# Optimization experiments

Hardware: AMD Instinct MI355X
Metric: run time of the kernel (lower is better)

Reference implementation:

```python
import jax, jax.numpy as jnp
import numpy as np

H, C, T = 4, 64, 6  # heads, per-head dim, num edge types


def segment_softmax(e, seg, n):
    # e: [E, H] logits, seg: [E] destination ids
    m = jax.ops.segment_max(e, seg, num_segments=n)
    m = jnp.where(jnp.isfinite(m), m, 0.0)
    w = jnp.exp(e - m[seg])
    s = jax.ops.segment_sum(w, seg, num_segments=n)
    return w / (s[seg] + 1e-16)


def gatv2(x_src, x_dst, ei, Wsrc, Wdst, att, b):
    # GATv2Conv (bipartite, add_self_loops=False, concat heads)
    n_dst = x_dst.shape[0]
    hs = (x_src @ Wsrc).reshape(x_src.shape[0], H, C)  # lin_l(x_src)
    hd = (x_dst @ Wdst).reshape(n_dst, H, C)            # lin_r(x_dst)
    src, dst = ei[0], ei[1]
    m = hs[src] + hd[dst]                                # [E,H,C]
    e = jnp.einsum('ehc,hc->eh', jax.nn.leaky_relu(m, 0.2), att)
    a = segment_softmax(e, dst, n_dst)                   # [E,H]
    out = jax.ops.segment_sum(a[:, :, None] * hs[src], dst, num_segments=n_dst)
    return out.reshape(n_dst, H * C) + b


def setup_inputs() -> dict:
    key = jax.random.key(0)
    ks = jax.random.split(key, 20)
    Npkg, N, Din, E, Dedge = 50000, 50000, 128, 200000, 8
    F = H * C  # 256
    K = T * Dedge  # num_clusters = 48 (forced by concat in subgraph_cls)
    s = 0.05
    return {
        'x_pkg': jax.random.normal(ks[0], (Npkg, Din), jnp.float32),
        'x_dst': jax.random.normal(ks[1], (T, N, Din), jnp.float32),
        'edge_attr': jax.random.uniform(ks[2], (T, E, Dedge), dtype=jnp.float32),
        'node_mask': jnp.ones((N,), jnp.float32),
        'W1_src': jax.random.normal(ks[3], (T, Din, F), jnp.float32) * s,
        'W1_dst': jax.random.normal(ks[4], (T, Din, F), jnp.float32) * s,
        'att1': jax.random.normal(ks[5], (T, H, C), jnp.float32) * s,
        'b1': jnp.zeros((T, F), jnp.float32),
        'W2_src': jax.random.normal(ks[6], (T, Din, F), jnp.float32) * s,
        'W2_dst': jax.random.normal(ks[7], (T, F, F), jnp.float32) * s,
        'att2': jax.random.normal(ks[8], (T, H, C), jnp.float32) * s,
        'b2': jnp.zeros((T, F), jnp.float32),
        'W_pool': jax.random.normal(ks[9], (F, K), jnp.float32) * s,
        'b_pool': jnp.zeros((K,), jnp.float32),
        'W_cls': jax.random.normal(ks[10], (F + 1, 1), jnp.float32) * s,
        'b_cls': jnp.zeros((1,), jnp.float32),
        'edge_index': jax.random.randint(ks[11], (T, 2, E), 0, N, dtype=jnp.int32),
        'batch': jnp.zeros((N,), jnp.int32),
    }


def reference(x_pkg, x_dst, edge_attr, node_mask, W1_src, W1_dst, att1, b1,
              W2_src, W2_dst, att2, b2, W_pool, b_pool, W_cls, b_cls,
              edge_index, batch):
    # node masking (edge_mask is all-ones -> bernoulli keeps every edge)
    xp = x_pkg * node_mask[:x_pkg.shape[0], None]
    outs = []
    for t in range(T):  # fixed set of 6 hetero edge types
        xd = x_dst[t] * node_mask[:x_dst.shape[1], None]
        h1 = jax.nn.relu(gatv2(xp, xd, edge_index[t], W1_src[t], W1_dst[t], att1[t], b1[t]))
        h2 = gatv2(xp, h1, edge_index[t], W2_src[t], W2_dst[t], att2[t], b2[t])
        outs.append(h2)
    h = outs[-1]  # forward keeps only the last node type's pooled embedding
    # DiffPool: soft assignment then pooled features
    s_assign = jax.nn.softmax(h @ W_pool + b_pool, axis=-1)  # [N, K]
    x_pooled = s_assign.T @ h                                 # [K, F]
    # global edge-attribute aggregation
    agg_edge = edge_attr.mean(axis=1).reshape(-1)             # [T*Dedge] == K
    feat = jnp.concatenate([x_pooled, agg_edge[:, None]], axis=-1)  # [K, F+1]
    return jax.nn.sigmoid(feat @ W_cls + b_cls)               # [K, 1]
```

## Files before the change

### kernel.cpp

```cpp
#include <hip/hip_runtime.h>
#include <math.h>

#define NN 50000
#define DIN 128
#define FDIM 256
#define EE 200000
#define TT 6
#define DE 8
#define KC 48
#define NB ((NN + 255)/256)

typedef __attribute__((ext_vector_type(8))) short bf16x8;
typedef __attribute__((ext_vector_type(8))) unsigned short u16x8;
typedef __attribute__((ext_vector_type(4))) float f32x4;

__device__ inline unsigned short f2b(float f){
  unsigned u = __float_as_uint(f);
  unsigned r = u + 0x7FFFu + ((u >> 16) & 1u);
  return (unsigned short)(r >> 16);
}
__device__ inline float b2f(unsigned short u){ return __uint_as_float(((unsigned)u) << 16); }

__global__ void zero_deg_agg(int* __restrict__ deg, int* __restrict__ aggE){
  int i = blockIdx.x*256 + threadIdx.x;
  if (i < NN) deg[i] = 0;
  if (i < 64) aggE[i] = 0;
}

__global__ void count_deg(const int* __restrict__ dst, int* __restrict__ deg){
  int i = blockIdx.x*256 + threadIdx.x;
  if (i < EE) atomicAdd(&deg[dst[i]], 1);
}

__global__ __launch_bounds__(256) void scan_blk(const int* __restrict__ deg, int* __restrict__ rp,
                                                int* __restrict__ bsum){
  __shared__ int sm[256];
  int i = blockIdx.x*256 + threadIdx.x;
  int v = (i < NN) ? deg[i] : 0;
  sm[threadIdx.x] = v;
  __syncthreads();
  #pragma unroll
  for (int off = 1; off < 256; off <<= 1){
    int t = (threadIdx.x >= (unsigned)off) ? sm[threadIdx.x - off] : 0;
    __syncthreads();
    sm[threadIdx.x] += t;
    __syncthreads();
  }
  if (i < NN) rp[i] = sm[threadIdx.x] - v;
  if (threadIdx.x == 255) bsum[blockIdx.x] = sm[255];
}

__global__ __launch_bounds__(256) void scan_sums(const int* __restrict__ bsum, int* __restrict__ boff){
  __shared__ int sm[256];
  int v = (threadIdx.x < NB) ? bsum[threadIdx.x] : 0;
  sm[threadIdx.x] = v;
  __syncthreads();
  #pragma unroll
  for (int off = 1; off < 256; off <<= 1){
    int t = (threadIdx.x >= (unsigned)off) ? sm[threadIdx.x - off] : 0;
    __syncthreads();
    sm[threadIdx.x] += t;
    __syncthreads();
  }
  if (threadIdx.x < NB) boff[threadIdx.x] = sm[threadIdx.x] - v;
}

__global__ __launch_bounds__(256) void scan_add(int* __restrict__ rp, const int* __restrict__ boff,
                                                int* __restrict__ cursor){
  int i = blockIdx.x*256 + threadIdx.x;
  if (i < NN){
    int r = rp[i] + boff[blockIdx.x];
    rp[i] = r;
    cursor[i] = r;
  }
  if (i == 0) rp[NN] = EE;
}

__global__ void scatter_edges(const int* __restrict__ src, const int* __restrict__ dst,
                              int* __restrict__ cursor, int* __restrict__ srt){
  int i = blockIdx.x*256 + threadIdx.x;
  if (i < EE){ int pos = atomicAdd(&cursor[dst[i]], 1); srt[pos] = src[i]; }
}

__global__ void cvt_wt_all(const float* __restrict__ W1s, const float* __restrict__ W2s,
                           const float* __restrict__ W1d, const float* __restrict__ W2d,
                           unsigned short* __restrict__ Wtall, unsigned short* __restrict__ Wt2d){
  int n = blockIdx.x;
  int which = blockIdx.y;
  if (which == 3){
    for (int k = threadIdx.x; k < FDIM; k += 256)
      Wt2d[(size_t)n*FDIM + k] = f2b(W2d[(size_t)k*256 + n]);
  } else {
    const float* W = (which == 0) ? W1s : (which == 1) ? W2s : W1d;
    unsigned short* o = Wtall + (size_t)which*256*DIN + (size_t)n*DIN;
    for (int k = threadIdx.x; k < DIN; k += 256)
      o[k] = f2b(W[(size_t)k*256 + n]);
  }
}

__global__ __launch_bounds__(256) void gemm_l1(const float* __restrict__ Apkg, const float* __restrict__ Adst,
                                               const unsigned short* __restrict__ Wtall,
                                               const float* __restrict__ mask,
                                               unsigned short* __restrict__ Chs1,
                                               unsigned short* __restrict__ Chs2,
                                               unsigned short* __restrict__ Chd1){
  __shared__ short Afull[128][136];
  __shared__ short Bl[128][56];
  int tid = threadIdx.x;
  int lane = tid & 63;
  int w = tid >> 6;
  int wm = w >> 1, wn = w & 1;
  int row0 = blockIdx.x * 128;
  int fr = lane & 15;
  int kb = lane >> 4;
  const float* A = blockIdx.y ? Adst : Apkg;
  #pragma unroll
  for (int p = 0; p < 8; p++){
    int idx = tid + p*256;
    int r = idx >> 4, ch = idx & 15;
    int gr = row0 + r;
    u16x8 o = (u16x8){0,0,0,0,0,0,0,0};
    if (gr < NN){
      float mv = mask[gr];
      const float* ap = A + (size_t)gr*DIN + ch*8;
      float4 a0 = *(const float4*)(ap);
      float4 a1 = *(const float4*)(ap + 4);
      o[0]=f2b(a0.x*mv); o[1]=f2b(a0.y*mv); o[2]=f2b(a0.z*mv); o[3]=f2b(a0.w*mv);
      o[4]=f2b(a1.x*mv); o[5]=f2b(a1.y*mv); o[6]=f2b(a1.z*mv); o[7]=f2b(a1.w*mv);
    }
    *(u16x8*)(&Afull[r][ch*8]) = o;
  }
  int ntile = blockIdx.y ? 2 : 4;
  #pragma unroll 1
  for (int t = 0; t < ntile; t++){
    int wsel = blockIdx.y ? 2 : (t >> 1);
    const unsigned short* Wt = Wtall + (size_t)wsel*256*DIN;
    unsigned short* Co = blockIdx.y ? Chd1 : ((t >> 1) ? Chs2 : Chs1);
    int col0 = (t & 1) * 128;
    f32x4 acc[4][4];
    #pragma unroll
    for (int i = 0; i < 4; i++)
      #pragma unroll
      for (int j = 0; j < 4; j++)
        acc[i][j] = (f32x4){0.f, 0.f, 0.f, 0.f};
    for (int k0 = 0; k0 < DIN; k0 += 32){
      bf16x8 rb[2];
      #pragma unroll
      for (int p = 0; p < 2; p++){
        int idx = tid + p*256;
        int r = idx >> 2, ch = idx & 3;
        rb[p] = *(const bf16x8*)(Wt + (size_t)(col0 + r)*DIN + k0 + ch*8);
      }
      __syncthreads();
      #pragma unroll
      for (int p = 0; p < 2; p++){
        int idx = tid + p*256;
        int r = idx >> 2, ch = idx & 3;
        *(bf16x8*)(&Bl[r][ch*8]) = rb[p];
      }
      __syncthreads();
      bf16x8 af[4], bfr[4];
      #pragma unroll
      for (int i = 0; i < 4; i++) af[i]  = *(const bf16x8*)(&Afull[wm*64 + i*16 + fr][k0 + kb*8]);
      #pragma unroll
      for (int j = 0; j < 4; j++) bfr[j] = *(const bf16x8*)(&Bl[wn*64 + j*16 + fr][kb*8]);
      #pragma unroll
      for (int i = 0; i < 4; i++)
        #pragma unroll
        for (int j = 0; j < 4; j++)
          acc[i][j] = __builtin_amdgcn_mfma_f32_16x16x32_bf16(af[i], bfr[j], acc[i][j], 0, 0, 0);
    }
    #pragma unroll
    for (int i = 0; i < 4; i++){
      #pragma unroll
      for (int q = 0; q < 4; q++){
        int grow = row0 + wm*64 + i*16 + kb*4 + q;
        if (grow < NN){
          #pragma unroll
          for (int j = 0; j < 4; j++)
            Co[(size_t)grow*256 + col0 + wn*64 + j*16 + fr] = f2b(acc[i][j][q]);
        }
      }
    }
  }
}

__global__ __launch_bounds__(256) void gemm_bf16(const short* __restrict__ A, const short* __restrict__ Wt,
                                                 unsigned short* __restrict__ Cb, int M, int K){
  __shared__ short Al[128][56];
  __shared__ short Bl[128][56];
  int tid = threadIdx.x;
  int lane = tid & 63;
  int w = tid >> 6;
  int wm = w >> 1, wn = w & 1;
  int row0 = blockIdx.x * 128, col0 = blockIdx.y * 128;
  int fr = lane & 15;
  int kb = lane >> 4;
  f32x4 acc[4][4];
  #pragma unroll
  for (int i = 0; i < 4; i++)
    #pragma unroll
    for (int j = 0; j < 4; j++)
      acc[i][j] = (f32x4){0.f, 0.f, 0.f, 0.f};

  for (int k0 = 0; k0 < K; k0 += 32){
    bf16x8 ra[2], rb[2];
    #pragma unroll
    for (int p = 0; p < 2; p++){
      int idx = tid + p*256;
      int r = idx >> 2, ch = idx & 3;
      int gr = row0 + r;
      if (gr < M) ra[p] = *(const bf16x8*)(A + (size_t)gr*K + k0 + ch*8);
      else        ra[p] = (bf16x8){0,0,0,0,0,0,0,0};
      rb[p] = *(const bf16x8*)(Wt + (size_t)(col0 + r)*K + k0 + ch*8);
    }
    __syncthreads();
    #pragma unroll
    for (int p = 0; p < 2; p++){
      int idx = tid + p*256;
      int r = idx >> 2, ch = idx & 3;
      *(bf16x8*)(&Al[r][ch*8]) = ra[p];
      *(bf16x8*)(&Bl[r][ch*8]) = rb[p];
    }
    __syncthreads();
    bf16x8 af[4], bfr[4];
    #pragma unroll
    for (int i = 0; i < 4; i++) af[i]  = *(const bf16x8*)(&Al[wm*64 + i*16 + fr][kb*8]);
    #pragma unroll
    for (int j = 0; j < 4; j++) bfr[j] = *(const bf16x8*)(&Bl[wn*64 + j*16 + fr][kb*8]);
    #pragma unroll
    for (int i = 0; i < 4; i++)
      #pragma unroll
      for (int j = 0; j < 4; j++)
        acc[i][j] = __builtin_amdgcn_mfma_f32_16x16x32_bf16(af[i], bfr[j], acc[i][j], 0, 0, 0);
  }
  #pragma unroll
  for (int i = 0; i < 4; i++){
    #pragma unroll
    for (int q = 0; q < 4; q++){
      int grow = row0 + wm*64 + i*16 + kb*4 + q;
      if (grow < M){
        #pragma unroll
        for (int j = 0; j < 4; j++)
          Cb[(size_t)grow*256 + col0 + wn*64 + j*16 + fr] = f2b(acc[i][j][q]);
      }
    }
  }
}

__global__ __launch_bounds__(256) void gat_fused(const int* __restrict__ rp, const int* __restrict__ srt,
                                                 const unsigned short* __restrict__ hs,
                                                 const unsigned short* __restrict__ hd,
                                                 const float* __restrict__ att, const float* __restrict__ bias,
                                                 unsigned short* __restrict__ outb, int do_relu){
  int n = blockIdx.x*4 + (threadIdx.x >> 6);
  int lane = threadIdx.x & 63;
  if (n >= NN) return;
  const float4 av = *(const float4*)(att + lane*4);
  ushort4 ud = *(const ushort4*)(hd + (size_t)n*256 + lane*4);
  float d0 = b2f(ud.x), d1 = b2f(ud.y), d2 = b2f(ud.z), d3 = b2f(ud.w);
  int beg = rp[n], end = rp[n+1];
  float4 acc = {0.f,0.f,0.f,0.f};
  float sw = 0.f;
  int i = beg;
  for (; i + 1 < end; i += 2){
    int sA = srt[i], sB = srt[i+1];
    ushort4 uA = *(const ushort4*)(hs + (size_t)sA*256 + lane*4);
    ushort4 uB = *(const ushort4*)(hs + (size_t)sB*256 + lane*4);
    float hA0 = b2f(uA.x), hA1 = b2f(uA.y), hA2 = b2f(uA.z), hA3 = b2f(uA.w);
    float hB0 = b2f(uB.x), hB1 = b2f(uB.y), hB2 = b2f(uB.z), hB3 = b2f(uB.w);
    float mA0 = hA0 + d0, mA1 = hA1 + d1, mA2 = hA2 + d2, mA3 = hA3 + d3;
    float mB0 = hB0 + d0, mB1 = hB1 + d1, mB2 = hB2 + d2, mB3 = hB3 + d3;
    mA0 = (mA0 > 0.f) ? mA0 : 0.2f*mA0;  mB0 = (mB0 > 0.f) ? mB0 : 0.2f*mB0;
    mA1 = (mA1 > 0.f) ? mA1 : 0.2f*mA1;  mB1 = (mB1 > 0.f) ? mB1 : 0.2f*mB1;
    mA2 = (mA2 > 0.f) ? mA2 : 0.2f*mA2;  mB2 = (mB2 > 0.f) ? mB2 : 0.2f*mB2;
    mA3 = (mA3 > 0.f) ? mA3 : 0.2f*mA3;  mB3 = (mB3 > 0.f) ? mB3 : 0.2f*mB3;
    float pA = mA0*av.x + mA1*av.y + mA2*av.z + mA3*av.w;
    float pB = mB0*av.x + mB1*av.y + mB2*av.z + mB3*av.w;
    #pragma unroll
    for (int msk = 8; msk > 0; msk >>= 1){
      pA += __shfl_xor(pA, msk);
      pB += __shfl_xor(pB, msk);
    }
    float wA = expf(fminf(pA, 80.f));
    float wB = expf(fminf(pB, 80.f));
    acc.x = fmaf(wA, hA0, fmaf(wB, hB0, acc.x));
    acc.y = fmaf(wA, hA1, fmaf(wB, hB1, acc.y));
    acc.z = fmaf(wA, hA2, fmaf(wB, hB2, acc.z));
    acc.w = fmaf(wA, hA3, fmaf(wB, hB3, acc.w));
    sw += wA + wB;
  }
  if (i < end){
    int s = srt[i];
    ushort4 uh = *(const ushort4*)(hs + (size_t)s*256 + lane*4);
    float h0 = b2f(uh.x), h1 = b2f(uh.y), h2 = b2f(uh.z), h3 = b2f(uh.w);
    float m0 = h0 + d0, m1 = h1 + d1, m2 = h2 + d2, m3 = h3 + d3;
    m0 = (m0 > 0.f) ? m0 : 0.2f*m0;
    m1 = (m1 > 0.f) ? m1 : 0.2f*m1;
    m2 = (m2 > 0.f) ? m2 : 0.2f*m2;
    m3 = (m3 > 0.f) ? m3 : 0.2f*m3;
    float p = m0*av.x + m1*av.y + m2*av.z + m3*av.w;
    #pragma unroll
    for (int msk = 8; msk > 0; msk >>= 1) p += __shfl_xor(p, msk);
    float wv = expf(fminf(p, 80.f));
    acc.x = fmaf(wv, h0, acc.x);
    acc.y = fmaf(wv, h1, acc.y);
    acc.z = fmaf(wv, h2, acc.z);
    acc.w = fmaf(wv, h3, acc.w);
    sw += wv;
  }
  float inv = 1.f / (sw + 1e-16f);
  const float4 b4 = *(const float4*)(bias + lane*4);
  float4 r;
  r.x = acc.x*inv + b4.x;
  r.y = acc.y*inv + b4.y;
  r.z = acc.z*inv + b4.z;
  r.w = acc.w*inv + b4.w;
  if (do_relu){
    r.x = fmaxf(r.x, 0.f); r.y = fmaxf(r.y, 0.f);
    r.z = fmaxf(r.z, 0.f); r.w = fmaxf(r.w, 0.f);
  }
  ushort4 o;
  o.x = f2b(r.x); o.y = f2b(r.y); o.z = f2b(r.z); o.w = f2b(r.w);
  *(ushort4*)(outb + (size_t)n*256 + lane*4) = o;
}

__global__ __launch_bounds__(256) void pool_logits_mfma(const unsigned short* __restrict__ h2b,
                                                        const float* __restrict__ Wp,
                                                        const float* __restrict__ bp,
                                                        unsigned short* __restrict__ sass,
                                                        float* __restrict__ xp){
  __shared__ short Al[128][56];
  __shared__ short Bn[KC][264];
  int tid = threadIdx.x;
  int lane = tid & 63;
  int w = tid >> 6;
  int row0 = blockIdx.x * 128;
  int fr = lane & 15;
  int kb = lane >> 4;
  if (blockIdx.x == 0){
    for (int i = tid; i < KC*FDIM; i += 256) xp[i] = 0.f;
  }
  for (int idx = tid; idx < 256*KC; idx += 256){
    int k = idx / KC, n = idx % KC;
    Bn[n][k] = f2b(Wp[idx]);
  }
  f32x4 acc[2][3];
  #pragma unroll
  for (int i = 0; i < 2; i++)
    #pragma unroll
    for (int j = 0; j < 3; j++)
      acc[i][j] = (f32x4){0.f, 0.f, 0.f, 0.f};

  for (int k0 = 0; k0 < 256; k0 += 32){
    bf16x8 ra[2];
    #pragma unroll
    for (int p = 0; p < 2; p++){
      int idx = tid + p*256;
      int r = idx >> 2, ch = idx & 3;
      int gr = row0 + r;
      if (gr < NN) ra[p] = *(const bf16x8*)((const short*)h2b + (size_t)gr*256 + k0 + ch*8);
      else         ra[p] = (bf16x8){0,0,0,0,0,0,0,0};
    }
    __syncthreads();
    #pragma unroll
    for (int p = 0; p < 2; p++){
      int idx = tid + p*256;
      int r = idx >> 2, ch = idx & 3;
      *(bf16x8*)(&Al[r][ch*8]) = ra[p];
    }
    __syncthreads();
    bf16x8 af[2], bfr[3];
    #pragma unroll
    for (int i = 0; i < 2; i++) af[i]  = *(const bf16x8*)(&Al[w*32 + i*16 + fr][kb*8]);
    #pragma unroll
    for (int j = 0; j < 3; j++) bfr[j] = *(const bf16x8*)(&Bn[j*16 + fr][k0 + kb*8]);
    #pragma unroll
    for (int i = 0; i < 2; i++)
      #pragma unroll
      for (int j = 0; j < 3; j++)
        acc[i][j] = __builtin_amdgcn_mfma_f32_16x16x32_bf16(af[i], bfr[j], acc[i][j], 0, 0, 0);
  }
  float bb[3];
  #pragma unroll
  for (int j = 0; j < 3; j++) bb[j] = bp[j*16 + fr];
  #pragma unroll
  for (int i = 0; i < 2; i++){
    #pragma unroll
    for (int q = 0; q < 4; q++){
      int grow = row0 + w*32 + i*16 + kb*4 + q;
      float v0 = acc[i][0][q] + bb[0];
      float v1 = acc[i][1][q] + bb[1];
      float v2 = acc[i][2][q] + bb[2];
      float m = fmaxf(v0, fmaxf(v1, v2));
      #pragma unroll
      for (int msk = 8; msk > 0; msk >>= 1) m = fmaxf(m, __shfl_xor(m, msk));
      float e0 = expf(v0 - m), e1 = expf(v1 - m), e2 = expf(v2 - m);
      float s = e0 + e1 + e2;
      #pragma unroll
      for (int msk = 8; msk > 0; msk >>= 1) s += __shfl_xor(s, msk);
      float inv = 1.f / s;
      if (grow < NN){
        unsigned short* so = sass + (size_t)grow*KC;
        so[fr]      = f2b(e0 * inv);
        so[16 + fr] = f2b(e1 * inv);
        so[32 + fr] = f2b(e2 * inv);
      }
    }
  }
}

#define PCH 64
#define NPART ((NN + PCH - 1)/PCH)
__global__ __launch_bounds__(256) void pooled_partial(const unsigned short* __restrict__ sass,
                                                      const unsigned short* __restrict__ h2b,
                                                      float* __restrict__ part){
  __shared__ float sld[PCH][KC];
  int t = threadIdx.x;
  int base = blockIdx.x * PCH;
  int cnt = min(PCH, NN - base);
  for (int idx = t; idx < cnt*KC; idx += 256)
    sld[idx/KC][idx%KC] = b2f(sass[(size_t)(base + idx/KC)*KC + idx%KC]);
  __syncthreads();
  float acc[KC];
  #pragma unroll
  for (int k = 0; k < KC; k++) acc[k] = 0.f;
  for (int n = 0; n < cnt; n++){
    float v = b2f(h2b[(size_t)(base + n)*256 + t]);
    #pragma unroll
    for (int k = 0; k < KC; k++) acc[k] = fmaf(sld[n][k], v, acc[k]);
  }
  float* po = part + (size_t)blockIdx.x*KC*256;
  #pragma unroll
  for (int k = 0; k < KC; k++) po[k*256 + t] = acc[k];
}

#define PSPL 8
__global__ __launch_bounds__(256) void pooled_reduce(const float* __restrict__ part, float* __restrict__ xp){
  int idx = blockIdx.x*256 + threadIdx.x;
  const int per = (NPART + PSPL - 1)/PSPL;
  int p0 = blockIdx.y * per;
  int p1 = min(p0 + per, NPART);
  float s0 = 0.f, s1 = 0.f;
  int p = p0;
  for (; p + 1 < p1; p += 2){
    s0 += part[(size_t)p*KC*256 + idx];
    s1 += part[(size_t)(p+1)*KC*256 + idx];
  }
  if (p < p1) s0 += part[(size_t)p*KC*256 + idx];
  atomicAdd(&xp[idx], s0 + s1);
}

#define BPT 128
__global__ __launch_bounds__(256) void edge_attr_mean(const float* __restrict__ ea, float* __restrict__ out){
  int t   = blockIdx.x / BPT;
  int blk = blockIdx.x % BPT;
  const int NF4 = EE * 2;
  const int per_blk = (NF4 + BPT - 1) / BPT;
  int i0 = blk * per_blk;
  int i1 = min(i0 + per_blk, NF4);
  const float4* base = (const float4*)(ea + (size_t)t*EE*DE);
  float s[8] = {0,0,0,0,0,0,0,0};
  for (int i = i0 + (int)threadIdx.x; i < i1; i += 256){
    float4 v = base[i];
    int db = (i & 1) * 4;
    s[db+0] += v.x; s[db+1] += v.y; s[db+2] += v.z; s[db+3] += v.w;
  }
  __shared__ float red[256];
  for (int d = 0; d < 8; d++){
    red[threadIdx.x] = s[d];
    __syncthreads();
    for (int off = 128; off > 0; off >>= 1){
      if (threadIdx.x < (unsigned)off) red[threadIdx.x] += red[threadIdx.x + off];
      __syncthreads();
    }
    if (threadIdx.x == 0) atomicAdd(&out[t*DE + d], red[0] / (float)EE);
    __syncthreads();
  }
}

__global__ void final_cls(const float* __restrict__ xp, const float* __restrict__ agg,
                          const float* __restrict__ Wc, const float* __restrict__ bc,
                          float* __restrict__ out){
  int k = threadIdx.x;
  if (k < KC){
    float s = bc[0];
    for (int f = 0; f < 256; f++) s = fmaf(xp[k*256 + f], Wc[f], s);
    s = fmaf(agg[k], Wc[256], s);
    out[k] = 1.f/(1.f + expf(-s));
  }
}

extern "C" void kernel_launch(void* const* d_in, const int* in_sizes, int n_in,
                              void* d_out, int out_size, void* d_ws, size_t ws_size,
                              hipStream_t stream) {
  const float* x_pkg     = (const float*)d_in[0];
  const float* x_dst     = (const float*)d_in[1];
  const float* edge_attr = (const float*)d_in[2];
  const float* node_mask = (const float*)d_in[3];
  const float* W1_src    = (const float*)d_in[4];
  const float* W1_dst    = (const float*)d_in[5];
  const float* att1      = (const float*)d_in[6];
  const float* b1        = (const float*)d_in[7];
  const float* W2_src    = (const float*)d_in[8];
  const float* W2_dst    = (const float*)d_in[9];
  const float* att2      = (const float*)d_in[10];
  const float* b2        = (const float*)d_in[11];
  const float* W_pool    = (const float*)d_in[12];
  const float* b_pool    = (const float*)d_in[13];
  const float* W_cls     = (const float*)d_in[14];
  const float* b_cls     = (const float*)d_in[15];
  const int*   edge_index= (const int*)d_in[16];
  float* out = (float*)d_out;

  const int T5 = TT - 1;
  const float* W1s5 = W1_src + (size_t)T5*DIN*FDIM;
  const float* W1d5 = W1_dst + (size_t)T5*DIN*FDIM;
  const float* a1_5 = att1   + (size_t)T5*FDIM;
  const float* b1_5 = b1     + (size_t)T5*FDIM;
  const float* W2s5 = W2_src + (size_t)T5*DIN*FDIM;
  const float* W2d5 = W2_dst + (size_t)T5*FDIM*FDIM;
  const float* a2_5 = att2   + (size_t)T5*FDIM;
  const float* b2_5 = b2     + (size_t)T5*FDIM;
  const float* xd5  = x_dst  + (size_t)T5*NN*DIN;
  const int* src5   = edge_index + (size_t)T5*2*EE;
  const int* dst5   = src5 + EE;

  float* buf0 = (float*)d_ws;
  float* buf1 = buf0 + (size_t)NN*FDIM;
  float* buf2 = buf1 + (size_t)NN*FDIM;
  float* xpool= buf2 + (size_t)NN*FDIM;
  float* aggE = xpool + KC*FDIM;
  int* deg    = (int*)(aggE + 64);
  int* rp     = deg + NN;
  int* cursor = rp + NN + 1;
  int* srt    = cursor + NN;
  unsigned short* Wtall = (unsigned short*)(srt + EE);
  unsigned short* Wt2d  = Wtall + (size_t)3*256*DIN;
  int* bsum = (int*)(Wt2d + (size_t)256*FDIM);
  int* boff = bsum + NB;
  unsigned short* hs1b = (unsigned short*)buf0;
  unsigned short* hs2b = hs1b + (size_t)NN*FDIM;
  unsigned short* hd1b = (unsigned short*)buf1;
  unsigned short* h1b  = hd1b + (size_t)NN*FDIM;
  unsigned short* h2b  = (unsigned short*)buf1;
  unsigned short* hd2b = (unsigned short*)buf2;
  unsigned short* sass = (unsigned short*)buf2;

  zero_deg_agg<<<(NN+255)/256, 256, 0, stream>>>(deg, (int*)aggE);
  count_deg<<<(EE+255)/256, 256, 0, stream>>>(dst5, deg);
  scan_blk<<<NB, 256, 0, stream>>>(deg, rp, bsum);
  scan_sums<<<1, 256, 0, stream>>>(bsum, boff);
  scan_add<<<NB, 256, 0, stream>>>(rp, boff, cursor);
  scatter_edges<<<(EE+255)/256, 256, 0, stream>>>(src5, dst5, cursor, srt);

  edge_attr_mean<<<TT*BPT, 256, 0, stream>>>(edge_attr, aggE);

  cvt_wt_all<<<dim3(256, 4), 256, 0, stream>>>(W1s5, W2s5, W1d5, W2d5, Wtall, Wt2d);

  gemm_l1<<<dim3((NN + 127)/128, 2), 256, 0, stream>>>(x_pkg, xd5, Wtall, node_mask,
                                                        hs1b, hs2b, hd1b);
  gat_fused<<<NN/4, 256, 0, stream>>>(rp, srt, hs1b, hd1b, a1_5, b1_5, h1b, 1);

  gemm_bf16<<<dim3((NN + 127)/128, 2), 256, 0, stream>>>((const short*)h1b, (const short*)Wt2d,
                                                          hd2b, NN, FDIM);
  gat_fused<<<NN/4, 256, 0, stream>>>(rp, srt, hs2b, hd2b, a2_5, b2_5, h2b, 0);

  pool_logits_mfma<<<(NN + 127)/128, 256, 0, stream>>>(h2b, W_pool, b_pool, sass, xpool);
  pooled_partial<<<NPART, 256, 0, stream>>>(sass, h2b, buf0);
  pooled_reduce<<<dim3(KC, PSPL), 256, 0, stream>>>(buf0, xpool);
  final_cls<<<1, 64, 0, stream>>>(xpool, aggE, W_cls, b_cls, out);
}
```

Baseline: 283.0 us.

## Merge small setup kernels, unroll GAT edge loop by four, halve pooled partials

Merges zeroing and weight conversion into one launch, and degree counting with the edge-attribute mean into another. The block-sum scan now runs inside scan_add, with each block reducing the prefix of the block sums itself. The GAT aggregation loop now handles four edges per iteration so more gathers are in flight. pooled_partial gives each block two chunks, which halves the partial buffer and the reduce work. Together these cut launch count and raise memory-level parallelism, at the cost of more registers in gat_fused and some redundant prefix work in scan_add.

```diff
diff --git a/kernel.cpp b/kernel.cpp
--- a/kernel.cpp
+++ b/kernel.cpp
@@ -9,6 +9,7 @@
 #define DE 8
 #define KC 48
 #define NB ((NN + 255)/256)
+#define CDB ((EE + 255)/256)
 
 typedef __attribute__((ext_vector_type(8))) short bf16x8;
 typedef __attribute__((ext_vector_type(8))) unsigned short u16x8;
@@ -21,15 +22,61 @@
 }
 __device__ inline float b2f(unsigned short u){ return __uint_as_float(((unsigned)u) << 16); }
 
-__global__ void zero_deg_agg(int* __restrict__ deg, int* __restrict__ aggE){
-  int i = blockIdx.x*256 + threadIdx.x;
-  if (i < NN) deg[i] = 0;
-  if (i < 64) aggE[i] = 0;
-}
-
-__global__ void count_deg(const int* __restrict__ dst, int* __restrict__ deg){
-  int i = blockIdx.x*256 + threadIdx.x;
-  if (i < EE) atomicAdd(&deg[dst[i]], 1);
+__global__ void init_misc(const float* __restrict__ W1s, const float* __restrict__ W2s,
+                          const float* __restrict__ W1d, const float* __restrict__ W2d,
+                          unsigned short* __restrict__ Wtall, unsigned short* __restrict__ Wt2d,
+                          int* __restrict__ deg, int* __restrict__ aggE){
+  int n = blockIdx.x;
+  int which = blockIdx.y;
+  if (which == 4){
+    int i = n*256 + threadIdx.x;
+    if (i < NN) deg[i] = 0;
+    if (i < 64) aggE[i] = 0;
+  } else if (which == 3){
+    for (int k = threadIdx.x; k < FDIM; k += 256)
+      Wt2d[(size_t)n*FDIM + k] = f2b(W2d[(size_t)k*256 + n]);
+  } else {
+    const float* W = (which == 0) ? W1s : (which == 1) ? W2s : W1d;
+    unsigned short* o = Wtall + (size_t)which*256*DIN + (size_t)n*DIN;
+    for (int k = threadIdx.x; k < DIN; k += 256)
+      o[k] = f2b(W[(size_t)k*256 + n]);
+  }
+}
+
+#define BPT 128
+__global__ __launch_bounds__(256) void count_and_mean(const int* __restrict__ dst, int* __restrict__ deg,
+                                                      const float* __restrict__ ea, float* __restrict__ aggE){
+  int b = blockIdx.x;
+  if (b < CDB){
+    int i = b*256 + threadIdx.x;
+    if (i < EE) atomicAdd(&deg[dst[i]], 1);
+    return;
+  }
+  int bb = b - CDB;
+  int t   = bb / BPT;
+  int blk = bb % BPT;
+  const int NF4 = EE * 2;
+  const int per_blk = (NF4 + BPT - 1) / BPT;
+  int i0 = blk * per_blk;
+  int i1 = min(i0 + per_blk, NF4);
+  const float4* base = (const float4*)(ea + (size_t)t*EE*DE);
+  float s[8] = {0,0,0,0,0,0,0,0};
+  for (int i = i0 + (int)threadIdx.x; i < i1; i += 256){
+    float4 v = base[i];
+    int db = (i & 1) * 4;
+    s[db+0] += v.x; s[db+1] += v.y; s[db+2] += v.z; s[db+3] += v.w;
+  }
+  __shared__ float red[256];
+  for (int d = 0; d < 8; d++){
+    red[threadIdx.x] = s[d];
+    __syncthreads();
+    for (int off = 128; off > 0; off >>= 1){
+      if (threadIdx.x < (unsigned)off) red[threadIdx.x] += red[threadIdx.x + off];
+      __syncthreads();
+    }
+    if (threadIdx.x == 0) atomicAdd(&aggE[t*DE + d], red[0] / (float)EE);
+    __syncthreads();
+  }
 }
 
 __global__ __launch_bounds__(256) void scan_blk(const int* __restrict__ deg, int* __restrict__ rp,
@@ -50,26 +97,21 @@
   if (threadIdx.x == 255) bsum[blockIdx.x] = sm[255];
 }
 
-__global__ __launch_bounds__(256) void scan_sums(const int* __restrict__ bsum, int* __restrict__ boff){
-  __shared__ int sm[256];
-  int v = (threadIdx.x < NB) ? bsum[threadIdx.x] : 0;
-  sm[threadIdx.x] = v;
+__global__ __launch_bounds__(256) void scan_add(int* __restrict__ rp, const int* __restrict__ bsum,
+                                                int* __restrict__ cursor){
+  __shared__ int red[256];
+  int t = threadIdx.x;
+  red[t] = (t < (int)blockIdx.x) ? bsum[t] : 0;
   __syncthreads();
   #pragma unroll
-  for (int off = 1; off < 256; off <<= 1){
-    int t = (threadIdx.x >= (unsigned)off) ? sm[threadIdx.x - off] : 0;
-    __syncthreads();
-    sm[threadIdx.x] += t;
-    __syncthreads();
-  }
-  if (threadIdx.x < NB) boff[threadIdx.x] = sm[threadIdx.x] - v;
-}
-
-__global__ __launch_bounds__(256) void scan_add(int* __restrict__ rp, const int* __restrict__ boff,
-                                                int* __restrict__ cursor){
-  int i = blockIdx.x*256 + threadIdx.x;
+  for (int off = 128; off > 0; off >>= 1){
+    if (t < off) red[t] += red[t + off];
+    __syncthreads();
+  }
+  int boffs = red[0];
+  int i = blockIdx.x*256 + t;
   if (i < NN){
-    int r = rp[i] + boff[blockIdx.x];
+    int r = rp[i] + boffs;
     rp[i] = r;
     cursor[i] = r;
   }
@@ -80,22 +122,6 @@
                               int* __restrict__ cursor, int* __restrict__ srt){
   int i = blockIdx.x*256 + threadIdx.x;
   if (i < EE){ int pos = atomicAdd(&cursor[dst[i]], 1); srt[pos] = src[i]; }
-}
-
-__global__ void cvt_wt_all(const float* __restrict__ W1s, const float* __restrict__ W2s,
-                           const float* __restrict__ W1d, const float* __restrict__ W2d,
-                           unsigned short* __restrict__ Wtall, unsigned short* __restrict__ Wt2d){
-  int n = blockIdx.x;
-  int which = blockIdx.y;
-  if (which == 3){
-    for (int k = threadIdx.x; k < FDIM; k += 256)
-      Wt2d[(size_t)n*FDIM + k] = f2b(W2d[(size_t)k*256 + n]);
-  } else {
-    const float* W = (which == 0) ? W1s : (which == 1) ? W2s : W1d;
-    unsigned short* o = Wtall + (size_t)which*256*DIN + (size_t)n*DIN;
-    for (int k = threadIdx.x; k < DIN; k += 256)
-      o[k] = f2b(W[(size_t)k*256 + n]);
-  }
 }
 
 __global__ __launch_bounds__(256) void gemm_l1(const float* __restrict__ Apkg, const float* __restrict__ Adst,
@@ -263,34 +289,44 @@
   float4 acc = {0.f,0.f,0.f,0.f};
   float sw = 0.f;
   int i = beg;
-  for (; i + 1 < end; i += 2){
-    int sA = srt[i], sB = srt[i+1];
+  for (; i + 3 < end; i += 4){
+    int sA = srt[i], sB = srt[i+1], sC = srt[i+2], sD = srt[i+3];
     ushort4 uA = *(const ushort4*)(hs + (size_t)sA*256 + lane*4);
     ushort4 uB = *(const ushort4*)(hs + (size_t)sB*256 + lane*4);
-    float hA0 = b2f(uA.x), hA1 = b2f(uA.y), hA2 = b2f(uA.z), hA3 = b2f(uA.w);
-    float hB0 = b2f(uB.x), hB1 = b2f(uB.y), hB2 = b2f(uB.z), hB3 = b2f(uB.w);
-    float mA0 = hA0 + d0, mA1 = hA1 + d1, mA2 = hA2 + d2, mA3 = hA3 + d3;
-    float mB0 = hB0 + d0, mB1 = hB1 + d1, mB2 = hB2 + d2, mB3 = hB3 + d3;
-    mA0 = (mA0 > 0.f) ? mA0 : 0.2f*mA0;  mB0 = (mB0 > 0.f) ? mB0 : 0.2f*mB0;
-    mA1 = (mA1 > 0.f) ? mA1 : 0.2f*mA1;  mB1 = (mB1 > 0.f) ? mB1 : 0.2f*mB1;
-    mA2 = (mA2 > 0.f) ? mA2 : 0.2f*mA2;  mB2 = (mB2 > 0.f) ? mB2 : 0.2f*mB2;
-    mA3 = (mA3 > 0.f) ? mA3 : 0.2f*mA3;  mB3 = (mB3 > 0.f) ? mB3 : 0.2f*mB3;
+    ushort4 uC = *(const ushort4*)(hs + (size_t)sC*256 + lane*4);
+    ushort4 uD = *(const ushort4*)(hs + (size_t)sD*256 + lane*4);
+    float hA0=b2f(uA.x), hA1=b2f(uA.y), hA2=b2f(uA.z), hA3=b2f(uA.w);
+    float hB0=b2f(uB.x), hB1=b2f(uB.y), hB2=b2f(uB.z), hB3=b2f(uB.w);
+    float hC0=b2f(uC.x), hC1=b2f(uC.y), hC2=b2f(uC.z), hC3=b2f(uC.w);
+    float hD0=b2f(uD.x), hD1=b2f(uD.y), hD2=b2f(uD.z), hD3=b2f(uD.w);
+    float mA0=hA0+d0, mA1=hA1+d1, mA2=hA2+d2, mA3=hA3+d3;
+    float mB0=hB0+d0, mB1=hB1+d1, mB2=hB2+d2, mB3=hB3+d3;
+    float mC0=hC0+d0, mC1=hC1+d1, mC2=hC2+d2, mC3=hC3+d3;
+    float mD0=hD0+d0, mD1=hD1+d1, mD2=hD2+d2, mD3=hD3+d3;
+    mA0=(mA0>0.f)?mA0:0.2f*mA0; mB0=(mB0>0.f)?mB0:0.2f*mB0; mC0=(mC0>0.f)?mC0:0.2f*mC0; mD0=(mD0>0.f)?mD0:0.2f*mD0;
+    mA1=(mA1>0.f)?mA1:0.2f*mA1; mB1=(mB1>0.f)?mB1:0.2f*mB1; mC1=(mC1>0.f)?mC1:0.2f*mC1; mD1=(mD1>0.f)?mD1:0.2f*mD1;
+    mA2=(mA2>0.f)?mA2:0.2f*mA2; mB2=(mB2>0.f)?mB2:0.2f*mB2; mC2=(mC2>0.f)?mC2:0.2f*mC2; mD2=(mD2>0.f)?mD2:0.2f*mD2;
+    mA3=(mA3>0.f)?mA3:0.2f*mA3; mB3=(mB3>0.f)?mB3:0.2f*mB3; mC3=(mC3>0.f)?mC3:0.2f*mC3; mD3=(mD3>0.f)?mD3:0.2f*mD3;
     float pA = mA0*av.x + mA1*av.y + mA2*av.z + mA3*av.w;
     float pB = mB0*av.x + mB1*av.y + mB2*av.z + mB3*av.w;
+    float pC = mC0*av.x + mC1*av.y + mC2*av.z + mC3*av.w;
+    float pD = mD0*av.x + mD1*av.y + mD2*av.z + mD3*av.w;
     #pragma unroll
     for (int msk = 8; msk > 0; msk >>= 1){
-      pA += __shfl_xor(pA, msk);
-      pB += __shfl_xor(pB, msk);
+      pA += __shfl_xor(pA, msk); pB += __shfl_xor(pB, msk);
+      pC += __shfl_xor(pC, msk); pD += __shfl_xor(pD, msk);
     }
     float wA = expf(fminf(pA, 80.f));
     float wB = expf(fminf(pB, 80.f));
-    acc.x = fmaf(wA, hA0, fmaf(wB, hB0, acc.x));
-    acc.y = fmaf(wA, hA1, fmaf(wB, hB1, acc.y));
-    acc.z = fmaf(wA, hA2, fmaf(wB, hB2, acc.z));
-    acc.w = fmaf(wA, hA3, fmaf(wB, hB3, acc.w));
-    sw += wA + wB;
-  }
-  if (i < end){
+    float wC = expf(fminf(pC, 80.f));
+    float wD = expf(fminf(pD, 80.f));
+    acc.x = fmaf(wA, hA0, fmaf(wB, hB0, fmaf(wC, hC0, fmaf(wD, hD0, acc.x))));
+    acc.y = fmaf(wA, hA1, fmaf(wB, hB1, fmaf(wC, hC1, fmaf(wD, hD1, acc.y))));
+    acc.z = fmaf(wA, hA2, fmaf(wB, hB2, fmaf(wC, hC2, fmaf(wD, hD2, acc.z))));
+    acc.w = fmaf(wA, hA3, fmaf(wB, hB3, fmaf(wC, hC3, fmaf(wD, hD3, acc.w))));
+    sw += (wA + wB) + (wC + wD);
+  }
+  for (; i < end; i++){
     int s = srt[i];
     ushort4 uh = *(const ushort4*)(hs + (size_t)s*256 + lane*4);
     float h0 = b2f(uh.x), h1 = b2f(uh.y), h2 = b2f(uh.z), h3 = b2f(uh.w);
@@ -411,24 +447,30 @@
 }
 
 #define PCH 64
-#define NPART ((NN + PCH - 1)/PCH)
+#define PPB 2
+#define NPART ((NN + PCH*PPB - 1)/(PCH*PPB))
 __global__ __launch_bounds__(256) void pooled_partial(const unsigned short* __restrict__ sass,
                                                       const unsigned short* __restrict__ h2b,
                                                       float* __restrict__ part){
   __shared__ float sld[PCH][KC];
   int t = threadIdx.x;
-  int base = blockIdx.x * PCH;
-  int cnt = min(PCH, NN - base);
-  for (int idx = t; idx < cnt*KC; idx += 256)
-    sld[idx/KC][idx%KC] = b2f(sass[(size_t)(base + idx/KC)*KC + idx%KC]);
-  __syncthreads();
   float acc[KC];
   #pragma unroll
   for (int k = 0; k < KC; k++) acc[k] = 0.f;
-  for (int n = 0; n < cnt; n++){
-    float v = b2f(h2b[(size_t)(base + n)*256 + t]);
-    #pragma unroll
-    for (int k = 0; k < KC; k++) acc[k] = fmaf(sld[n][k], v, acc[k]);
+  #pragma unroll 1
+  for (int c = 0; c < PPB; c++){
+    int base = (blockIdx.x*PPB + c) * PCH;
+    if (base >= NN) break;
+    int cnt = min(PCH, NN - base);
+    __syncthreads();
+    for (int idx = t; idx < cnt*KC; idx += 256)
+      sld[idx/KC][idx%KC] = b2f(sass[(size_t)(base + idx/KC)*KC + idx%KC]);
+    __syncthreads();
+    for (int n = 0; n < cnt; n++){
+      float v = b2f(h2b[(size_t)(base + n)*256 + t]);
+      #pragma unroll
+      for (int k = 0; k < KC; k++) acc[k] = fmaf(sld[n][k], v, acc[k]);
+    }
   }
   float* po = part + (size_t)blockIdx.x*KC*256;
   #pragma unroll
@@ -449,34 +491,6 @@
   }
   if (p < p1) s0 += part[(size_t)p*KC*256 + idx];
   atomicAdd(&xp[idx], s0 + s1);
-}
-
-#define BPT 128
-__global__ __launch_bounds__(256) void edge_attr_mean(const float* __restrict__ ea, float* __restrict__ out){
-  int t   = blockIdx.x / BPT;
-  int blk = blockIdx.x % BPT;
-  const int NF4 = EE * 2;
-  const int per_blk = (NF4 + BPT - 1) / BPT;
-  int i0 = blk * per_blk;
-  int i1 = min(i0 + per_blk, NF4);
-  const float4* base = (const float4*)(ea + (size_t)t*EE*DE);
-  float s[8] = {0,0,0,0,0,0,0,0};
-  for (int i = i0 + (int)threadIdx.x; i < i1; i += 256){
-    float4 v = base[i];
-    int db = (i & 1) * 4;
-    s[db+0] += v.x; s[db+1] += v.y; s[db+2] += v.z; s[db+3] += v.w;
-  }
-  __shared__ float red[256];
-  for (int d = 0; d < 8; d++){
-    red[threadIdx.x] = s[d];
-    __syncthreads();
-    for (int off = 128; off > 0; off >>= 1){
-      if (threadIdx.x < (unsigned)off) red[threadIdx.x] += red[threadIdx.x + off];
-      __syncthreads();
-    }
-    if (threadIdx.x == 0) atomicAdd(&out[t*DE + d], red[0] / (float)EE);
-    __syncthreads();
-  }
 }
 
 __global__ void final_cls(const float* __restrict__ xp, const float* __restrict__ agg,
@@ -538,7 +552,6 @@
   unsigned short* Wtall = (unsigned short*)(srt + EE);
   unsigned short* Wt2d  = Wtall + (size_t)3*256*DIN;
   int* bsum = (int*)(Wt2d + (size_t)256*FDIM);
-  int* boff = bsum + NB;
   unsigned short* hs1b = (unsigned short*)buf0;
   unsigned short* hs2b = hs1b + (size_t)NN*FDIM;
   unsigned short* hd1b = (unsigned short*)buf1;
@@ -547,16 +560,11 @@
   unsigned short* hd2b = (unsigned short*)buf2;
   unsigned short* sass = (unsigned short*)buf2;
 
-  zero_deg_agg<<<(NN+255)/256, 256, 0, stream>>>(deg, (int*)aggE);
-  count_deg<<<(EE+255)/256, 256, 0, stream>>>(dst5, deg);
+  init_misc<<<dim3(256, 5), 256, 0, stream>>>(W1s5, W2s5, W1d5, W2d5, Wtall, Wt2d, deg, (int*)aggE);
+  count_and_mean<<<CDB + TT*BPT, 256, 0, stream>>>(dst5, deg, edge_attr, aggE);
   scan_blk<<<NB, 256, 0, stream>>>(deg, rp, bsum);
-  scan_sums<<<1, 256, 0, stream>>>(bsum, boff);
-  scan_add<<<NB, 256, 0, stream>>>(rp, boff, cursor);
+  scan_add<<<NB, 256, 0, stream>>>(rp, bsum, cursor);
   scatter_edges<<<(EE+255)/256, 256, 0, stream>>>(src5, dst5, cursor, srt);
-
-  edge_attr_mean<<<TT*BPT, 256, 0, stream>>>(edge_attr, aggE);
-
-  cvt_wt_all<<<dim3(256, 4), 256, 0, stream>>>(W1s5, W2s5, W1d5, W2d5, Wtall, Wt2d);
 
   gemm_l1<<<dim3((NN + 127)/128, 2), 256, 0, stream>>>(x_pkg, xd5, Wtall, node_mask,
                                                         hs1b, hs2b, hd1b);
```

Measured after the change: 310.4 us. 1.1x slower.
